# Kernel optimization log

Hardware: AMD Instinct MI355X
Metric: run time of the kernel (lower is better)

The kernel has to match this reference:

```python
import jax, jax.numpy as jnp
import numpy as np

G = 256          # grid resolution -> V = G*G vertices
B = 8            # batch of meshes
N_SAMPLES = 2048
W_CHAMFER, W_EDGE, W_NORMAL, W_LAP = 1.0, 1.0, 0.1, 0.1
V = G * G


def _grid_faces(g):
    idx = np.arange(g * g).reshape(g, g)
    v00 = idx[:-1, :-1].ravel(); v01 = idx[:-1, 1:].ravel()
    v10 = idx[1:, :-1].ravel();  v11 = idx[1:, 1:].ravel()
    f1 = np.stack([v00, v01, v10], 1)
    f2 = np.stack([v01, v11, v10], 1)
    return np.concatenate([f1, f2], 0).astype(np.int32)  # [F,3]


def _edges_and_pairs(faces, n_verts):
    # all face-edge incidences + the opposite vertex of each incidence
    e = np.concatenate([faces[:, [0, 1]], faces[:, [1, 2]], faces[:, [0, 2]]], 0)
    opp = np.concatenate([faces[:, 2], faces[:, 0], faces[:, 1]], 0)
    e = np.sort(e, 1)
    key = e[:, 0].astype(np.int64) * n_verts + e[:, 1]
    order = np.argsort(key, kind='stable')
    key_s, es, opps = key[order], e[order], opp[order]
    first = np.ones(len(key_s), bool); first[1:] = key_s[1:] != key_s[:-1]
    edges = es[first].astype(np.int32)                      # unique undirected edges [E,2]
    dup = np.nonzero(~first)[0]                             # 2nd incidence of shared edges
    pairs = np.stack([es[dup - 1, 0], es[dup - 1, 1], opps[dup - 1], opps[dup]], 1).astype(np.int32)  # [P,4]
    return edges, pairs


def setup_inputs() -> dict:
    key = jax.random.key(0)
    faces = _grid_faces(G)
    edges, nc_pairs = _edges_and_pairs(faces, V)
    # base grid geometry + gaussian perturbation (realistic smooth-ish surfaces)
    xs, ys = np.meshgrid(np.linspace(0, 1, G), np.linspace(0, 1, G), indexing='ij')
    base = np.stack([xs, ys, 0.1 * np.sin(4 * np.pi * xs) * np.cos(4 * np.pi * ys)], -1).reshape(V, 3)
    k1, k2 = jax.random.split(key)
    verts_pred = jnp.asarray(base, jnp.float32)[None] + 0.01 * jax.random.normal(k1, (B, V, 3), jnp.float32)
    verts_targ = jnp.asarray(base, jnp.float32)[None] + 0.01 * jax.random.normal(k2, (B, V, 3), jnp.float32)
    return {
        'verts_pred': verts_pred,
        'verts_targ': verts_targ,
        'faces': jnp.asarray(faces),
        'edges': jnp.asarray(edges),
        'nc_pairs': jnp.asarray(nc_pairs),
    }


def _sample_points(verts, faces, key, n):
    # verts [V,3]; area-weighted face sampling + uniform barycentric (pytorch3d scheme)
    v0, v1, v2 = verts[faces[:, 0]], verts[faces[:, 1]], verts[faces[:, 2]]
    areas = 0.5 * jnp.linalg.norm(jnp.cross(v1 - v0, v2 - v0), axis=-1)          # [F]
    kf, kb = jax.random.split(key)
    fidx = jax.random.categorical(kf, jnp.log(areas + 1e-12), shape=(n,))        # [n]
    uv = jax.random.uniform(kb, (n, 2), verts.dtype)
    su = jnp.sqrt(uv[:, 0:1]); vv = uv[:, 1:2]
    w0, w1, w2 = 1.0 - su, su * (1.0 - vv), su * vv
    return w0 * v0[fidx] + w1 * v1[fidx] + w2 * v2[fidx]                         # [n,3]


def _chamfer(x, y):
    # squared-distance chamfer, mean over points then batch, both directions summed
    d = jnp.sum((x[:, :, None, :] - y[:, None, :, :]) ** 2, -1)                  # [B,N,M]
    return jnp.mean(jnp.min(d, axis=2)) + jnp.mean(jnp.min(d, axis=1))


def _edge_loss(verts, edges):
    diff = verts[:, edges[:, 0]] - verts[:, edges[:, 1]]                          # [B,E,3]
    return jnp.mean(jnp.sum(diff * diff, -1))                                     # (||e|| - 0)^2


def _normal_consistency(verts, nc_pairs):
    v0 = verts[:, nc_pairs[:, 0]]; v1 = verts[:, nc_pairs[:, 1]]
    a = verts[:, nc_pairs[:, 2]]; b = verts[:, nc_pairs[:, 3]]
    e = v1 - v0
    n0 = jnp.cross(e, a - v0)
    n1 = -jnp.cross(e, b - v0)
    eps = 1e-8
    cos = jnp.sum(n0 * n1, -1) / (
        jnp.maximum(jnp.linalg.norm(n0, axis=-1), eps)
        * jnp.maximum(jnp.linalg.norm(n1, axis=-1), eps))
    return jnp.mean(1.0 - cos)


def _laplacian_uniform(verts, edges):
    e0, e1 = edges[:, 0], edges[:, 1]
    ones = jnp.ones((edges.shape[0],), verts.dtype)

    def per_mesh(v):  # v [V,3]
        nsum = (jax.ops.segment_sum(v[e1], e0, num_segments=V)
                + jax.ops.segment_sum(v[e0], e1, num_segments=V))
        deg = (jax.ops.segment_sum(ones, e0, num_segments=V)
               + jax.ops.segment_sum(ones, e1, num_segments=V))
        lap = nsum / jnp.maximum(deg, 1.0)[:, None] - v                           # D^-1 A v - v
        return jnp.mean(jnp.linalg.norm(lap, axis=-1))

    return jnp.mean(jax.vmap(per_mesh)(verts))


def reference(verts_pred, verts_targ, faces, edges, nc_pairs):
    skey = jax.random.key(42)
    kp = jax.random.split(jax.random.fold_in(skey, 0), verts_pred.shape[0])
    kt = jax.random.split(jax.random.fold_in(skey, 1), verts_targ.shape[0])
    sample_pred = jax.vmap(lambda v, k: _sample_points(v, faces, k, N_SAMPLES))(verts_pred, kp)
    sample_targ = jax.vmap(lambda v, k: _sample_points(v, faces, k, N_SAMPLES))(verts_targ, kt)
    loss_chamfer = _chamfer(sample_pred, sample_targ)
    loss_edge = _edge_loss(verts_pred, edges)
    loss_normal = _normal_consistency(verts_pred, nc_pairs)
    loss_lap = _laplacian_uniform(verts_pred, edges)
    loss = (W_CHAMFER * loss_chamfer + W_EDGE * loss_edge
            + W_NORMAL * loss_normal + W_LAP * loss_lap)
    return (loss, loss_chamfer, loss_edge, loss_normal, loss_lap)
```

## Files before the change

### kernel.cpp

```cpp
#include <hip/hip_runtime.h>
#include <stdint.h>

#define GSZ 256
#define NV (GSZ*GSZ)
#define NS 2048
#define CELLS (255*255)
#define FH CELLS
#define NF (2*CELLS)
#define CH 8

#define EH 65280
#define EV 65280
#define PH 64770
#define PV 64770

struct F3 { float x, y, z; };

__device__ __forceinline__ F3 ldv3(const float* __restrict__ p, int idx) {
    const float* q = p + 3*(size_t)idx;
    F3 r; r.x = q[0]; r.y = q[1]; r.z = q[2]; return r;
}
__device__ __forceinline__ F3 f3sub(F3 a, F3 b) { return F3{a.x-b.x, a.y-b.y, a.z-b.z}; }
__device__ __forceinline__ F3 f3cross(F3 a, F3 b) {
    return F3{a.y*b.z - a.z*b.y, a.z*b.x - a.x*b.z, a.x*b.y - a.y*b.x};
}
__device__ __forceinline__ float f3dot(F3 a, F3 b) { return a.x*b.x + a.y*b.y + a.z*b.z; }

__device__ __forceinline__ uint64_t splitmix64(uint64_t& s) {
    s += 0x9E3779B97F4A7C15ULL;
    uint64_t z = s;
    z = (z ^ (z >> 30)) * 0xBF58476D1CE4E5B9ULL;
    z = (z ^ (z >> 27)) * 0x94D049BB133111EBULL;
    return z ^ (z >> 31);
}

__device__ __forceinline__ float blockReduceSum256(float v) {
    __shared__ float s[4];
    int lane = threadIdx.x & 63, w = threadIdx.x >> 6;
    #pragma unroll
    for (int o = 32; o > 0; o >>= 1) v += __shfl_down(v, o, 64);
    if (lane == 0) s[w] = v;
    __syncthreads();
    if (threadIdx.x == 0) v = s[0] + s[1] + s[2] + s[3];
    return v;
}

__global__ void k_area(const float* __restrict__ vp, const float* __restrict__ vt,
                       int B, float* __restrict__ areas, float* __restrict__ blockmax,
                       unsigned* __restrict__ counter) {
    if (blockIdx.x == 0 && threadIdx.x == 0) *counter = 0u;
    int gid = blockIdx.x*256 + threadIdx.x;
    int total = 2*B*CELLS;
    float mloc = 0.f;
    if (gid < total) {
        int m = gid / CELLS;
        int c = gid - m*CELLS;
        int i = c / 255, j = c - i*255;
        const float* verts = (m < B ? vp + (size_t)m*NV*3
                                    : vt + (size_t)(m-B)*NV*3);
        int b00 = i*GSZ + j;
        F3 v00 = ldv3(verts, b00);
        F3 v01 = ldv3(verts, b00+1);
        F3 v10 = ldv3(verts, b00+GSZ);
        F3 v11 = ldv3(verts, b00+GSZ+1);
        F3 c1 = f3cross(f3sub(v01, v00), f3sub(v10, v00));
        F3 c2 = f3cross(f3sub(v11, v01), f3sub(v10, v01));
        float a1 = 0.5f * sqrtf(f3dot(c1, c1));
        float a2 = 0.5f * sqrtf(f3dot(c2, c2));
        size_t base = (size_t)m*NF;
        areas[base + c]      = a1;
        areas[base + FH + c] = a2;
        mloc = fmaxf(a1, a2);
    }
    #pragma unroll
    for (int o = 32; o > 0; o >>= 1) mloc = fmaxf(mloc, __shfl_down(mloc, o, 64));
    __shared__ float s[4];
    int lane = threadIdx.x & 63, w = threadIdx.x >> 6;
    if (lane == 0) s[w] = mloc;
    __syncthreads();
    if (threadIdx.x == 0)
        blockmax[blockIdx.x] = fmaxf(fmaxf(s[0], s[1]), fmaxf(s[2], s[3]));
}

__global__ void k_sample(const float* __restrict__ vp, const float* __restrict__ vt,
                         int B, const float* __restrict__ areas,
                         const float* __restrict__ blockmax, int nbm,
                         float4* __restrict__ samples) {
    float m = 0.f;
    for (int k = threadIdx.x; k < nbm; k += 256) m = fmaxf(m, blockmax[k]);
    #pragma unroll
    for (int o = 32; o > 0; o >>= 1) m = fmaxf(m, __shfl_down(m, o, 64));
    __shared__ float s[4];
    int lane = threadIdx.x & 63, w = threadIdx.x >> 6;
    if (lane == 0) s[w] = m;
    __syncthreads();
    __shared__ float sMaxA;
    if (threadIdx.x == 0) sMaxA = fmaxf(fmaxf(s[0], s[1]), fmaxf(s[2], s[3]));
    __syncthreads();
    float maxA = sMaxA;

    int gid = blockIdx.x*256 + threadIdx.x;
    int cloud = gid / (B*NS);
    int rem = gid - cloud*(B*NS);
    int b = rem / NS;
    const float* verts = (cloud ? vt : vp) + (size_t)b*NV*3;
    const float* am = areas + (size_t)(cloud*B + b)*NF;

    uint64_t st = ((uint64_t)(gid + 1) * 0x9E3779B97F4A7C15ULL) ^ 0xC0FFEE123456789ULL;
    int f = 0;
    for (int round = 0; round < 64; ++round) {
        uint64_t r0 = splitmix64(st), r1 = splitmix64(st);
        uint64_t r2 = splitmix64(st), r3 = splitmix64(st);
        int f0 = (int)(((uint64_t)(uint32_t)r0 * (uint32_t)NF) >> 32);
        int f1 = (int)(((uint64_t)(uint32_t)r1 * (uint32_t)NF) >> 32);
        int f2 = (int)(((uint64_t)(uint32_t)r2 * (uint32_t)NF) >> 32);
        int f3 = (int)(((uint64_t)(uint32_t)r3 * (uint32_t)NF) >> 32);
        float a0 = am[f0], a1 = am[f1], a2 = am[f2], a3 = am[f3];
        float u0 = ((uint32_t)(r0 >> 40)) * (1.f/16777216.f);
        float u1 = ((uint32_t)(r1 >> 40)) * (1.f/16777216.f);
        float u2 = ((uint32_t)(r2 >> 40)) * (1.f/16777216.f);
        float u3 = ((uint32_t)(r3 >> 40)) * (1.f/16777216.f);
        if (u0 * maxA <= a0) { f = f0; break; }
        if (u1 * maxA <= a1) { f = f1; break; }
        if (u2 * maxA <= a2) { f = f2; break; }
        if (u3 * maxA <= a3) { f = f3; break; }
        f = f3;
    }
    int i0, i1, i2;
    if (f < FH) {
        int c = f;  int i = c / 255, j = c - i*255;  int v = i*GSZ + j;
        i0 = v; i1 = v + 1; i2 = v + GSZ;
    } else {
        int c = f - FH;  int i = c / 255, j = c - i*255;  int v = i*GSZ + j;
        i0 = v + 1; i1 = v + GSZ + 1; i2 = v + GSZ;
    }
    F3 v0 = ldv3(verts, i0), v1 = ldv3(verts, i1), v2 = ldv3(verts, i2);
    uint64_t r = splitmix64(st);
    float u0 = ((uint32_t)r >> 8) * (1.f/16777216.f);
    float u1 = ((uint32_t)(r >> 32) >> 8) * (1.f/16777216.f);
    float su = sqrtf(u0);
    float w0 = 1.f - su, w1 = su * (1.f - u1), w2 = su * u1;
    float X = w0*v0.x + w1*v1.x + w2*v2.x;
    float Y = w0*v0.y + w1*v1.y + w2*v2.y;
    float Z = w0*v0.z + w1*v1.z + w2*v2.z;
    samples[gid] = make_float4(X, Y, Z, X*X + Y*Y + Z*Z);
}

__global__ void k_heavy(const float* __restrict__ vp,
                        const float4* __restrict__ samples,
                        int B, int E, int P, int nbE, int nbP,
                        float* __restrict__ minpart,
                        float* __restrict__ partE, float* __restrict__ partP,
                        float* __restrict__ partV) {
    int bx = blockIdx.x, b = blockIdx.y;
    if (bx < 64) {
        int xh = bx >> 5, z = bx & 31;
        int dir = z >> 4, q = z & 15;
        const float4* src = samples + ((size_t)dir*B + b)*NS;
        const float4* dst = samples + ((size_t)(1-dir)*B + b)*NS;

        __shared__ float4 tile[128];
        if (threadIdx.x < 128) tile[threadIdx.x] = dst[q*128 + threadIdx.x];

        float nx[4], ny[4], nz[4], xx[4], mn[4];
        #pragma unroll
        for (int k = 0; k < 4; ++k) {
            int i = xh*1024 + k*256 + threadIdx.x;
            float4 sp = src[i];
            nx[k] = -2.f*sp.x; ny[k] = -2.f*sp.y; nz[k] = -2.f*sp.z;
            xx[k] = sp.w;
            mn[k] = 3.402823466e38f;
        }
        __syncthreads();
        #pragma unroll 4
        for (int j = 0; j < 128; ++j) {
            float4 t = tile[j];
            #pragma unroll
            for (int k = 0; k < 4; ++k) {
                float d = fmaf(nx[k], t.x, t.w);
                d = fmaf(ny[k], t.y, d);
                d = fmaf(nz[k], t.z, d);
                mn[k] = fminf(mn[k], d);
            }
        }
        float* outp = minpart + (((size_t)(dir*B + b)*16) + q)*NS;
        #pragma unroll
        for (int k = 0; k < 4; ++k)
            outp[xh*1024 + k*256 + threadIdx.x] = mn[k] + xx[k];
        return;
    }

    int mx = bx - 64;
    const float* verts = vp + (size_t)b*NV*3;
    float acc = 0.f;
    if (mx < nbE) {
        int base = mx*(256*CH);
        for (int c = 0; c < CH; ++c) {
            int e = base + c*256 + threadIdx.x;
            if (e < E) {
                int i0, i1;
                if (e < EH) {
                    int r = e / 255, cc = e - r*255;
                    i0 = r*GSZ + cc; i1 = i0 + 1;
                } else if (e < EH + EV) {
                    int e2 = e - EH;
                    int i = e2 >> 8, j = e2 & 255;
                    i0 = i*GSZ + j; i1 = i0 + GSZ;
                } else {
                    int e2 = e - (EH + EV);
                    int i = e2 / 255, j = e2 - i*255;
                    i0 = i*GSZ + j + 1; i1 = (i+1)*GSZ + j;
                }
                F3 d = f3sub(ldv3(verts, i0), ldv3(verts, i1));
                acc += f3dot(d, d);
            }
        }
        float s = blockReduceSum256(acc);
        if (threadIdx.x == 0) partE[(size_t)mx*B + b] = s;
    } else if (mx < nbE + nbP) {
        int base = (mx - nbE)*(256*CH);
        for (int c = 0; c < CH; ++c) {
            int p = base + c*256 + threadIdx.x;
            if (p < P) {
                int iv0, iv1, ia, ib;
                if (p < PH) {
                    int r = p / 255 + 1, cc = p - (r-1)*255;
                    iv0 = r*GSZ + cc; iv1 = iv0 + 1;
                    ia = iv0 + GSZ;
                    ib = iv0 - GSZ + 1;
                } else if (p < PH + PV) {
                    int p2 = p - PH;
                    int r = p2 / 254, j = p2 - r*254 + 1;
                    iv0 = r*GSZ + j; iv1 = iv0 + GSZ;
                    ia = iv0 + 1;
                    ib = iv0 + GSZ - 1;
                } else {
                    int p2 = p - (PH + PV);
                    int i = p2 / 255, j = p2 - i*255;
                    iv0 = i*GSZ + j + 1;
                    iv1 = (i+1)*GSZ + j;
                    ia = i*GSZ + j;
                    ib = (i+1)*GSZ + j + 1;
                }
                F3 v0 = ldv3(verts, iv0), v1 = ldv3(verts, iv1);
                F3 a = ldv3(verts, ia), bb = ldv3(verts, ib);
                F3 e = f3sub(v1, v0);
                F3 n0 = f3cross(e, f3sub(a, v0));
                F3 n1 = f3cross(f3sub(bb, v0), e);
                float num = f3dot(n0, n1);
                float den2 = fmaxf(f3dot(n0, n0), 1e-16f) * fmaxf(f3dot(n1, n1), 1e-16f);
                acc += 1.f - num * rsqrtf(den2);
            }
        }
        float s = blockReduceSum256(acc);
        if (threadIdx.x == 0) partP[(size_t)(mx - nbE)*B + b] = s;
    } else {
        int base = (mx - nbE - nbP)*(256*CH);
        for (int c = 0; c < CH; ++c) {
            int idx = base + c*256 + threadIdx.x;
            int i = idx >> 8, j = idx & 255;
            F3 ctr = ldv3(verts, idx);
            float nx = 0.f, ny = 0.f, nz = 0.f; int deg = 0;
            #define ADDN(ii, jj) { F3 n_ = ldv3(verts, (ii)*GSZ + (jj)); \
                                   nx += n_.x; ny += n_.y; nz += n_.z; ++deg; }
            if (j > 0)               ADDN(i, j-1);
            if (j < GSZ-1)           ADDN(i, j+1);
            if (i > 0)               ADDN(i-1, j);
            if (i < GSZ-1)           ADDN(i+1, j);
            if (i < GSZ-1 && j > 0)  ADDN(i+1, j-1);
            if (i > 0 && j < GSZ-1)  ADDN(i-1, j+1);
            #undef ADDN
            float inv = 1.f / (float)deg;
            float lx = nx*inv - ctr.x, ly = ny*inv - ctr.y, lz = nz*inv - ctr.z;
            acc += sqrtf(lx*lx + ly*ly + lz*lz);
        }
        float s = blockReduceSum256(acc);
        if (threadIdx.x == 0) partV[(size_t)(mx - nbE - nbP)*B + b] = s;
    }
}

__global__ void k_redfin(const float* __restrict__ minpart, int B,
                         const float* __restrict__ partE, int nE,
                         const float* __restrict__ partP, int nP,
                         const float* __restrict__ partV, int nL,
                         int E, int P,
                         float* __restrict__ chamPart,
                         unsigned* __restrict__ counter,
                         float* __restrict__ out) {
    int gid = blockIdx.x*256 + threadIdx.x;
    int dir = gid / (B*NS);
    int rem = gid - dir*(B*NS);
    int b = rem / NS, i = rem - b*NS;
    const float* p = minpart + (size_t)(dir*B + b)*16*NS + i;
    float mn = 3.402823466e38f;
    #pragma unroll
    for (int q = 0; q < 16; ++q) mn = fminf(mn, p[(size_t)q*NS]);
    float sm = blockReduceSum256(mn);
    if (threadIdx.x == 0) chamPart[blockIdx.x] = sm;

    __shared__ unsigned sTicket;
    if (threadIdx.x == 0) {
        __threadfence();
        sTicket = atomicAdd(counter, 1u);
    }
    __syncthreads();
    if (sTicket != (unsigned)(gridDim.x - 1)) return;
    __threadfence();

    const volatile float* cp = chamPart;
    double a0 = 0, a1 = 0, aE = 0, aP = 0, aL = 0;
    for (int k = threadIdx.x; k < 64;  k += 256) a0 += (double)cp[k];
    for (int k = 64 + threadIdx.x; k < 128; k += 256) a1 += (double)cp[k];
    for (int k = threadIdx.x; k < nE; k += 256) aE += (double)partE[k];
    for (int k = threadIdx.x; k < nP; k += 256) aP += (double)partP[k];
    for (int k = threadIdx.x; k < nL; k += 256) aL += (double)partV[k];
    __shared__ double sd[5][4];
    double v[5] = {a0, a1, aE, aP, aL};
    int lane = threadIdx.x & 63, w = threadIdx.x >> 6;
    #pragma unroll
    for (int r = 0; r < 5; ++r) {
        double x = v[r];
        #pragma unroll
        for (int o = 32; o > 0; o >>= 1) x += __shfl_down(x, o, 64);
        if (lane == 0) sd[r][w] = x;
    }
    __syncthreads();
    if (threadIdx.x == 0) {
        double bn = (double)B * NS;
        double ch = (sd[0][0]+sd[0][1]+sd[0][2]+sd[0][3]) / bn
                  + (sd[1][0]+sd[1][1]+sd[1][2]+sd[1][3]) / bn;
        double ed = (sd[2][0]+sd[2][1]+sd[2][2]+sd[2][3]) / ((double)B * E);
        double no = (sd[3][0]+sd[3][1]+sd[3][2]+sd[3][3]) / ((double)B * P);
        double la = (sd[4][0]+sd[4][1]+sd[4][2]+sd[4][3]) / ((double)B * NV);
        double loss = ch + ed + 0.1*no + 0.1*la;
        out[0] = (float)loss; out[1] = (float)ch; out[2] = (float)ed;
        out[3] = (float)no;   out[4] = (float)la;
    }
}

extern "C" void kernel_launch(void* const* d_in, const int* in_sizes, int n_in,
                              void* d_out, int out_size, void* d_ws, size_t ws_size,
                              hipStream_t stream) {
    const float* vp = (const float*)d_in[0];
    const float* vt = (const float*)d_in[1];
    const int B = in_sizes[0] / (3*NV);
    const int E = in_sizes[3] / 2;
    const int P = in_sizes[4] / 4;

    char* ws = (char*)d_ws;
    size_t off = 0;
    auto alloc = [&](size_t bytes) -> void* {
        void* p = ws + off;
        off = (off + bytes + 255) & ~(size_t)255;
        return p;
    };
    float*    areas    = (float*)   alloc((size_t)2*B*NF*sizeof(float));
    float4*   samples  = (float4*)  alloc((size_t)2*B*NS*sizeof(float4));
    float*    minpart  = (float*)   alloc((size_t)2*B*16*NS*sizeof(float));
    float*    blockmax = (float*)   alloc(8192*sizeof(float));
    float*    chamPart = (float*)   alloc(256*sizeof(float));
    float*    partE    = (float*)   alloc(2048*sizeof(float));
    float*    partP    = (float*)   alloc(2048*sizeof(float));
    float*    partV    = (float*)   alloc(1024*sizeof(float));
    unsigned* counter  = (unsigned*)alloc(256);

    int nbm = (2*B*CELLS + 255)/256;
    k_area<<<nbm, 256, 0, stream>>>(vp, vt, B, areas, blockmax, counter);
    k_sample<<<(2*B*NS)/256, 256, 0, stream>>>(vp, vt, B, areas, blockmax, nbm, samples);
    int nbE = (E + 256*CH - 1)/(256*CH);
    int nbP = (P + 256*CH - 1)/(256*CH);
    int nbV = NV/(256*CH);
    dim3 gh(64 + nbE + nbP + nbV, B);
    k_heavy<<<gh, 256, 0, stream>>>(vp, samples, B, E, P, nbE, nbP,
                                    minpart, partE, partP, partV);
    k_redfin<<<(2*B*NS)/256, 256, 0, stream>>>(minpart, B, partE, nbE*B,
                                               partP, nbP*B, partV, nbV*B,
                                               E, P, chamPart, counter,
                                               (float*)d_out);
}
```

Before: 136.9 us.

## Fuse chamfer min-reduction and final loss accumulation into heavy kernel

Removes the separate reduce/finalize kernel launch. The last of the 16 chamfer blocks per mesh/direction, chosen by an atomic ticket counter, takes the min over the partials and writes a per-mesh sum. The globally last block of the grid then computes the final losses. Each chamfer block now handles all 2048 source points with 8 per thread instead of 4, which halves the chamfer block count. This trades one launch and a pass over minpart for serialized tail work in the last-arriving blocks.

```diff
diff --git a/kernel.cpp b/kernel.cpp
--- a/kernel.cpp
+++ b/kernel.cpp
@@ -47,8 +47,8 @@
 
 __global__ void k_area(const float* __restrict__ vp, const float* __restrict__ vt,
                        int B, float* __restrict__ areas, float* __restrict__ blockmax,
-                       unsigned* __restrict__ counter) {
-    if (blockIdx.x == 0 && threadIdx.x == 0) *counter = 0u;
+                       unsigned* __restrict__ ctrl) {
+    if (blockIdx.x == 0 && threadIdx.x < 32) ctrl[threadIdx.x] = 0u;
     int gid = blockIdx.x*256 + threadIdx.x;
     int total = 2*B*CELLS;
     float mloc = 0.f;
@@ -146,196 +146,209 @@
     samples[gid] = make_float4(X, Y, Z, X*X + Y*Y + Z*Z);
 }
 
+__device__ __forceinline__ void final_accum(const float* chamPart, int nCh,
+                                            const float* partE, int nE,
+                                            const float* partP, int nP,
+                                            const float* partV, int nL,
+                                            int B, int E, int P, float* out) {
+    const volatile float* cp = chamPart;
+    const volatile float* pe = partE;
+    const volatile float* pp = partP;
+    const volatile float* pv = partV;
+    double aC = 0, aE = 0, aP = 0, aL = 0;
+    for (int k = threadIdx.x; k < nCh; k += 256) aC += (double)cp[k];
+    for (int k = threadIdx.x; k < nE;  k += 256) aE += (double)pe[k];
+    for (int k = threadIdx.x; k < nP;  k += 256) aP += (double)pp[k];
+    for (int k = threadIdx.x; k < nL;  k += 256) aL += (double)pv[k];
+    __shared__ double sd[4][4];
+    double v[4] = {aC, aE, aP, aL};
+    int lane = threadIdx.x & 63, w = threadIdx.x >> 6;
+    #pragma unroll
+    for (int r = 0; r < 4; ++r) {
+        double x = v[r];
+        #pragma unroll
+        for (int o = 32; o > 0; o >>= 1) x += __shfl_down(x, o, 64);
+        if (lane == 0) sd[r][w] = x;
+    }
+    __syncthreads();
+    if (threadIdx.x == 0) {
+        double bn = (double)B * NS;
+        double ch = (sd[0][0]+sd[0][1]+sd[0][2]+sd[0][3]) / bn;
+        double ed = (sd[1][0]+sd[1][1]+sd[1][2]+sd[1][3]) / ((double)B * E);
+        double no = (sd[2][0]+sd[2][1]+sd[2][2]+sd[2][3]) / ((double)B * P);
+        double la = (sd[3][0]+sd[3][1]+sd[3][2]+sd[3][3]) / ((double)B * NV);
+        double loss = ch + ed + 0.1*no + 0.1*la;
+        out[0] = (float)loss; out[1] = (float)ch; out[2] = (float)ed;
+        out[3] = (float)no;   out[4] = (float)la;
+    }
+}
+
 __global__ void k_heavy(const float* __restrict__ vp,
                         const float4* __restrict__ samples,
                         int B, int E, int P, int nbE, int nbP,
                         float* __restrict__ minpart,
                         float* __restrict__ partE, float* __restrict__ partP,
-                        float* __restrict__ partV) {
+                        float* __restrict__ partV,
+                        float* __restrict__ chamPart,
+                        unsigned* __restrict__ ctrl,
+                        float* __restrict__ out) {
     int bx = blockIdx.x, b = blockIdx.y;
-    if (bx < 64) {
-        int xh = bx >> 5, z = bx & 31;
-        int dir = z >> 4, q = z & 15;
+    int totalBlocks = gridDim.x * gridDim.y;
+
+    if (bx < 32) {
+        int dir = bx >> 4, q = bx & 15;
+        int g = dir*B + b;
         const float4* src = samples + ((size_t)dir*B + b)*NS;
         const float4* dst = samples + ((size_t)(1-dir)*B + b)*NS;
 
         __shared__ float4 tile[128];
         if (threadIdx.x < 128) tile[threadIdx.x] = dst[q*128 + threadIdx.x];
 
-        float nx[4], ny[4], nz[4], xx[4], mn[4];
+        float nx[8], ny[8], nz[8], xx[8], mn[8];
         #pragma unroll
-        for (int k = 0; k < 4; ++k) {
-            int i = xh*1024 + k*256 + threadIdx.x;
-            float4 sp = src[i];
+        for (int k = 0; k < 8; ++k) {
+            float4 sp = src[k*256 + threadIdx.x];
             nx[k] = -2.f*sp.x; ny[k] = -2.f*sp.y; nz[k] = -2.f*sp.z;
             xx[k] = sp.w;
             mn[k] = 3.402823466e38f;
         }
         __syncthreads();
-        #pragma unroll 4
+        #pragma unroll 2
         for (int j = 0; j < 128; ++j) {
             float4 t = tile[j];
             #pragma unroll
-            for (int k = 0; k < 4; ++k) {
+            for (int k = 0; k < 8; ++k) {
                 float d = fmaf(nx[k], t.x, t.w);
                 d = fmaf(ny[k], t.y, d);
                 d = fmaf(nz[k], t.z, d);
                 mn[k] = fminf(mn[k], d);
             }
         }
-        float* outp = minpart + (((size_t)(dir*B + b)*16) + q)*NS;
+        float* outp = minpart + ((size_t)g*16 + q)*NS;
         #pragma unroll
-        for (int k = 0; k < 4; ++k)
-            outp[xh*1024 + k*256 + threadIdx.x] = mn[k] + xx[k];
-        return;
-    }
-
-    int mx = bx - 64;
-    const float* verts = vp + (size_t)b*NV*3;
-    float acc = 0.f;
-    if (mx < nbE) {
-        int base = mx*(256*CH);
-        for (int c = 0; c < CH; ++c) {
-            int e = base + c*256 + threadIdx.x;
-            if (e < E) {
-                int i0, i1;
-                if (e < EH) {
-                    int r = e / 255, cc = e - r*255;
-                    i0 = r*GSZ + cc; i1 = i0 + 1;
-                } else if (e < EH + EV) {
-                    int e2 = e - EH;
-                    int i = e2 >> 8, j = e2 & 255;
-                    i0 = i*GSZ + j; i1 = i0 + GSZ;
-                } else {
-                    int e2 = e - (EH + EV);
-                    int i = e2 / 255, j = e2 - i*255;
-                    i0 = i*GSZ + j + 1; i1 = (i+1)*GSZ + j;
+        for (int k = 0; k < 8; ++k)
+            outp[k*256 + threadIdx.x] = mn[k] + xx[k];
+
+        __threadfence();
+        __syncthreads();
+        __shared__ unsigned tk;
+        if (threadIdx.x == 0) tk = atomicAdd(&ctrl[1+g], 1u);
+        __syncthreads();
+        if (tk == 15u) {
+            __threadfence();
+            float acc = 0.f;
+            const float* mp = minpart + (size_t)g*16*NS;
+            #pragma unroll
+            for (int kk = 0; kk < 8; ++kk) {
+                int i = kk*256 + threadIdx.x;
+                float m = 3.402823466e38f;
+                #pragma unroll
+                for (int q2 = 0; q2 < 16; ++q2)
+                    m = fminf(m, mp[(size_t)q2*NS + i]);
+                acc += m;
+            }
+            float s = blockReduceSum256(acc);
+            if (threadIdx.x == 0) chamPart[g] = s;
+        }
+    } else {
+        int mx = bx - 32;
+        const float* verts = vp + (size_t)b*NV*3;
+        float acc = 0.f;
+        if (mx < nbE) {
+            int base = mx*(256*CH);
+            for (int c = 0; c < CH; ++c) {
+                int e = base + c*256 + threadIdx.x;
+                if (e < E) {
+                    int i0, i1;
+                    if (e < EH) {
+                        int r = e / 255, cc = e - r*255;
+                        i0 = r*GSZ + cc; i1 = i0 + 1;
+                    } else if (e < EH + EV) {
+                        int e2 = e - EH;
+                        int i = e2 >> 8, j = e2 & 255;
+                        i0 = i*GSZ + j; i1 = i0 + GSZ;
+                    } else {
+                        int e2 = e - (EH + EV);
+                        int i = e2 / 255, j = e2 - i*255;
+                        i0 = i*GSZ + j + 1; i1 = (i+1)*GSZ + j;
+                    }
+                    F3 d = f3sub(ldv3(verts, i0), ldv3(verts, i1));
+                    acc += f3dot(d, d);
                 }
-                F3 d = f3sub(ldv3(verts, i0), ldv3(verts, i1));
-                acc += f3dot(d, d);
-            }
+            }
+            float s = blockReduceSum256(acc);
+            if (threadIdx.x == 0) partE[(size_t)mx*B + b] = s;
+        } else if (mx < nbE + nbP) {
+            int base = (mx - nbE)*(256*CH);
+            for (int c = 0; c < CH; ++c) {
+                int p = base + c*256 + threadIdx.x;
+                if (p < P) {
+                    int iv0, iv1, ia, ib;
+                    if (p < PH) {
+                        int r = p / 255 + 1, cc = p - (r-1)*255;
+                        iv0 = r*GSZ + cc; iv1 = iv0 + 1;
+                        ia = iv0 + GSZ;
+                        ib = iv0 - GSZ + 1;
+                    } else if (p < PH + PV) {
+                        int p2 = p - PH;
+                        int r = p2 / 254, j = p2 - r*254 + 1;
+                        iv0 = r*GSZ + j; iv1 = iv0 + GSZ;
+                        ia = iv0 + 1;
+                        ib = iv0 + GSZ - 1;
+                    } else {
+                        int p2 = p - (PH + PV);
+                        int i = p2 / 255, j = p2 - i*255;
+                        iv0 = i*GSZ + j + 1;
+                        iv1 = (i+1)*GSZ + j;
+                        ia = i*GSZ + j;
+                        ib = (i+1)*GSZ + j + 1;
+                    }
+                    F3 v0 = ldv3(verts, iv0), v1 = ldv3(verts, iv1);
+                    F3 a = ldv3(verts, ia), bb = ldv3(verts, ib);
+                    F3 e = f3sub(v1, v0);
+                    F3 n0 = f3cross(e, f3sub(a, v0));
+                    F3 n1 = f3cross(f3sub(bb, v0), e);
+                    float num = f3dot(n0, n1);
+                    float den2 = fmaxf(f3dot(n0, n0), 1e-16f) * fmaxf(f3dot(n1, n1), 1e-16f);
+                    acc += 1.f - num * rsqrtf(den2);
+                }
+            }
+            float s = blockReduceSum256(acc);
+            if (threadIdx.x == 0) partP[(size_t)(mx - nbE)*B + b] = s;
+        } else {
+            int base = (mx - nbE - nbP)*(256*CH);
+            for (int c = 0; c < CH; ++c) {
+                int idx = base + c*256 + threadIdx.x;
+                int i = idx >> 8, j = idx & 255;
+                F3 ctr = ldv3(verts, idx);
+                float nx = 0.f, ny = 0.f, nz = 0.f; int deg = 0;
+                #define ADDN(ii, jj) { F3 n_ = ldv3(verts, (ii)*GSZ + (jj)); \
+                                       nx += n_.x; ny += n_.y; nz += n_.z; ++deg; }
+                if (j > 0)               ADDN(i, j-1);
+                if (j < GSZ-1)           ADDN(i, j+1);
+                if (i > 0)               ADDN(i-1, j);
+                if (i < GSZ-1)           ADDN(i+1, j);
+                if (i < GSZ-1 && j > 0)  ADDN(i+1, j-1);
+                if (i > 0 && j < GSZ-1)  ADDN(i-1, j+1);
+                #undef ADDN
+                float inv = 1.f / (float)deg;
+                float lx = nx*inv - ctr.x, ly = ny*inv - ctr.y, lz = nz*inv - ctr.z;
+                acc += sqrtf(lx*lx + ly*ly + lz*lz);
+            }
+            float s = blockReduceSum256(acc);
+            if (threadIdx.x == 0) partV[(size_t)(mx - nbE - nbP)*B + b] = s;
         }
-        float s = blockReduceSum256(acc);
-        if (threadIdx.x == 0) partE[(size_t)mx*B + b] = s;
-    } else if (mx < nbE + nbP) {
-        int base = (mx - nbE)*(256*CH);
-        for (int c = 0; c < CH; ++c) {
-            int p = base + c*256 + threadIdx.x;
-            if (p < P) {
-                int iv0, iv1, ia, ib;
-                if (p < PH) {
-                    int r = p / 255 + 1, cc = p - (r-1)*255;
-                    iv0 = r*GSZ + cc; iv1 = iv0 + 1;
-                    ia = iv0 + GSZ;
-                    ib = iv0 - GSZ + 1;
-                } else if (p < PH + PV) {
-                    int p2 = p - PH;
-                    int r = p2 / 254, j = p2 - r*254 + 1;
-                    iv0 = r*GSZ + j; iv1 = iv0 + GSZ;
-                    ia = iv0 + 1;
-                    ib = iv0 + GSZ - 1;
-                } else {
-                    int p2 = p - (PH + PV);
-                    int i = p2 / 255, j = p2 - i*255;
-                    iv0 = i*GSZ + j + 1;
-                    iv1 = (i+1)*GSZ + j;
-                    ia = i*GSZ + j;
-                    ib = (i+1)*GSZ + j + 1;
-                }
-                F3 v0 = ldv3(verts, iv0), v1 = ldv3(verts, iv1);
-                F3 a = ldv3(verts, ia), bb = ldv3(verts, ib);
-                F3 e = f3sub(v1, v0);
-                F3 n0 = f3cross(e, f3sub(a, v0));
-                F3 n1 = f3cross(f3sub(bb, v0), e);
-                float num = f3dot(n0, n1);
-                float den2 = fmaxf(f3dot(n0, n0), 1e-16f) * fmaxf(f3dot(n1, n1), 1e-16f);
-                acc += 1.f - num * rsqrtf(den2);
-            }
-        }
-        float s = blockReduceSum256(acc);
-        if (threadIdx.x == 0) partP[(size_t)(mx - nbE)*B + b] = s;
-    } else {
-        int base = (mx - nbE - nbP)*(256*CH);
-        for (int c = 0; c < CH; ++c) {
-            int idx = base + c*256 + threadIdx.x;
-            int i = idx >> 8, j = idx & 255;
-            F3 ctr = ldv3(verts, idx);
-            float nx = 0.f, ny = 0.f, nz = 0.f; int deg = 0;
-            #define ADDN(ii, jj) { F3 n_ = ldv3(verts, (ii)*GSZ + (jj)); \
-                                   nx += n_.x; ny += n_.y; nz += n_.z; ++deg; }
-            if (j > 0)               ADDN(i, j-1);
-            if (j < GSZ-1)           ADDN(i, j+1);
-            if (i > 0)               ADDN(i-1, j);
-            if (i < GSZ-1)           ADDN(i+1, j);
-            if (i < GSZ-1 && j > 0)  ADDN(i+1, j-1);
-            if (i > 0 && j < GSZ-1)  ADDN(i-1, j+1);
-            #undef ADDN
-            float inv = 1.f / (float)deg;
-            float lx = nx*inv - ctr.x, ly = ny*inv - ctr.y, lz = nz*inv - ctr.z;
-            acc += sqrtf(lx*lx + ly*ly + lz*lz);
-        }
-        float s = blockReduceSum256(acc);
-        if (threadIdx.x == 0) partV[(size_t)(mx - nbE - nbP)*B + b] = s;
-    }
-}
-
-__global__ void k_redfin(const float* __restrict__ minpart, int B,
-                         const float* __restrict__ partE, int nE,
-                         const float* __restrict__ partP, int nP,
-                         const float* __restrict__ partV, int nL,
-                         int E, int P,
-                         float* __restrict__ chamPart,
-                         unsigned* __restrict__ counter,
-                         float* __restrict__ out) {
-    int gid = blockIdx.x*256 + threadIdx.x;
-    int dir = gid / (B*NS);
-    int rem = gid - dir*(B*NS);
-    int b = rem / NS, i = rem - b*NS;
-    const float* p = minpart + (size_t)(dir*B + b)*16*NS + i;
-    float mn = 3.402823466e38f;
-    #pragma unroll
-    for (int q = 0; q < 16; ++q) mn = fminf(mn, p[(size_t)q*NS]);
-    float sm = blockReduceSum256(mn);
-    if (threadIdx.x == 0) chamPart[blockIdx.x] = sm;
-
-    __shared__ unsigned sTicket;
-    if (threadIdx.x == 0) {
-        __threadfence();
-        sTicket = atomicAdd(counter, 1u);
-    }
-    __syncthreads();
-    if (sTicket != (unsigned)(gridDim.x - 1)) return;
+    }
+
     __threadfence();
-
-    const volatile float* cp = chamPart;
-    double a0 = 0, a1 = 0, aE = 0, aP = 0, aL = 0;
-    for (int k = threadIdx.x; k < 64;  k += 256) a0 += (double)cp[k];
-    for (int k = 64 + threadIdx.x; k < 128; k += 256) a1 += (double)cp[k];
-    for (int k = threadIdx.x; k < nE; k += 256) aE += (double)partE[k];
-    for (int k = threadIdx.x; k < nP; k += 256) aP += (double)partP[k];
-    for (int k = threadIdx.x; k < nL; k += 256) aL += (double)partV[k];
-    __shared__ double sd[5][4];
-    double v[5] = {a0, a1, aE, aP, aL};
-    int lane = threadIdx.x & 63, w = threadIdx.x >> 6;
-    #pragma unroll
-    for (int r = 0; r < 5; ++r) {
-        double x = v[r];
-        #pragma unroll
-        for (int o = 32; o > 0; o >>= 1) x += __shfl_down(x, o, 64);
-        if (lane == 0) sd[r][w] = x;
-    }
-    __syncthreads();
-    if (threadIdx.x == 0) {
-        double bn = (double)B * NS;
-        double ch = (sd[0][0]+sd[0][1]+sd[0][2]+sd[0][3]) / bn
-                  + (sd[1][0]+sd[1][1]+sd[1][2]+sd[1][3]) / bn;
-        double ed = (sd[2][0]+sd[2][1]+sd[2][2]+sd[2][3]) / ((double)B * E);
-        double no = (sd[3][0]+sd[3][1]+sd[3][2]+sd[3][3]) / ((double)B * P);
-        double la = (sd[4][0]+sd[4][1]+sd[4][2]+sd[4][3]) / ((double)B * NV);
-        double loss = ch + ed + 0.1*no + 0.1*la;
-        out[0] = (float)loss; out[1] = (float)ch; out[2] = (float)ed;
-        out[3] = (float)no;   out[4] = (float)la;
-    }
+    __syncthreads();
+    __shared__ unsigned gt;
+    if (threadIdx.x == 0) gt = atomicAdd(&ctrl[0], 1u);
+    __syncthreads();
+    if (gt != (unsigned)(totalBlocks - 1)) return;
+    __threadfence();
+    final_accum(chamPart, 2*B, partE, nbE*B, partP, nbP*B, partV,
+                (NV/(256*CH))*B, B, E, P, out);
 }
 
 extern "C" void kernel_launch(void* const* d_in, const int* in_sizes, int n_in,
@@ -362,19 +375,16 @@
     float*    partE    = (float*)   alloc(2048*sizeof(float));
     float*    partP    = (float*)   alloc(2048*sizeof(float));
     float*    partV    = (float*)   alloc(1024*sizeof(float));
-    unsigned* counter  = (unsigned*)alloc(256);
+    unsigned* ctrl     = (unsigned*)alloc(256);
 
     int nbm = (2*B*CELLS + 255)/256;
-    k_area<<<nbm, 256, 0, stream>>>(vp, vt, B, areas, blockmax, counter);
+    k_area<<<nbm, 256, 0, stream>>>(vp, vt, B, areas, blockmax, ctrl);
     k_sample<<<(2*B*NS)/256, 256, 0, stream>>>(vp, vt, B, areas, blockmax, nbm, samples);
     int nbE = (E + 256*CH - 1)/(256*CH);
     int nbP = (P + 256*CH - 1)/(256*CH);
     int nbV = NV/(256*CH);
-    dim3 gh(64 + nbE + nbP + nbV, B);
+    dim3 gh(32 + nbE + nbP + nbV, B);
     k_heavy<<<gh, 256, 0, stream>>>(vp, samples, B, E, P, nbE, nbP,
-                                    minpart, partE, partP, partV);
-    k_redfin<<<(2*B*NS)/256, 256, 0, stream>>>(minpart, B, partE, nbE*B,
-                                               partP, nbP*B, partV, nbV*B,
-                                               E, P, chamPart, counter,
-                                               (float*)d_out);
-}
+                                    minpart, partE, partP, partV,
+                                    chamPart, ctrl, (float*)d_out);
+}
```

Result: slower. 295.6 us (+115.9%).
